# Performance work log

Measured on AMD Instinct MI355X. Metric: run time of the kernel, lower is better.

The kernel has to match this reference:

```python
import jax, jax.numpy as jnp
import numpy as np

EPS = 1e-8      # torch F.cosine_similarity eps
MARGIN = 0.6
POS_MASK = 2.0  # added at the positive location before top-k mining
K_NEG = 4


def setup_inputs() -> dict:
    key = jax.random.key(0)
    k1, k2, k3, k4 = jax.random.split(key, 4)
    B, C, H, W = 4, 256, 64, 64
    sketch = jax.random.normal(k1, (B, C, H, W), dtype=jnp.float32)
    ref = jax.random.normal(k2, (B, C, H, W), dtype=jnp.float32)
    # one anchor coordinate per positive grid cell (B*H*W pairs total)
    anchor_y = jax.random.randint(k3, (B, H * W), 0, H, dtype=jnp.int32)
    anchor_x = jax.random.randint(k4, (B, H * W), 0, W, dtype=jnp.int32)
    return {"sketch_query_vectors": sketch, "ref_key_vectors": ref,
            "anchor_y": anchor_y, "anchor_x": anchor_x}


def reference(sketch_query_vectors, ref_key_vectors, anchor_y, anchor_x):
    B, C, H, W = sketch_query_vectors.shape
    M = H * W  # ref locations; also number of positive pairs per batch elem

    sketch_flat = sketch_query_vectors.reshape(B, C, M)  # (B, C, M)
    ref_flat = ref_key_vectors.reshape(B, C, M)          # (B, C, M)

    # gather anchor features at (anchor_y, anchor_x): flat index ay*W + ax
    a_idx = anchor_y * W + anchor_x                      # (B, N), N == M
    anchors = jnp.take_along_axis(sketch_flat, a_idx[:, None, :], axis=2)  # (B, C, N)
    anchors = anchors.transpose(0, 2, 1)                 # (B, N, C)

    # cosine similarity of each anchor vs full ref map of same batch elem
    dot = jnp.einsum('bnc,bcm->bnm', anchors, ref_flat)  # (B, N, M)
    a_norm = jnp.linalg.norm(anchors, axis=-1)           # (B, N)
    r_norm = jnp.linalg.norm(ref_flat, axis=1)           # (B, M)
    sim = dot / jnp.maximum(a_norm[:, :, None] * r_norm[:, None, :], EPS)
    dist = 1.0 - sim                                     # (B, N, M)

    # positive location for pair n is grid cell n -> diagonal
    pos_distance = jnp.mean(jnp.diagonal(dist, axis1=1, axis2=2))

    # mask the positive location then mine 4 smallest distances
    masked = dist + POS_MASK * jnp.eye(M, dtype=dist.dtype)[None, :, :]
    neg_vals = -jax.lax.top_k(-masked, K_NEG)[0]         # (B, N, K_NEG)
    neg_loss = jnp.mean(jnp.maximum(MARGIN - neg_vals, 0.0))

    return pos_distance + neg_loss
```

## Files before the change

kernel.cpp:

```cpp
#include <hip/hip_runtime.h>
#include <math.h>

#define B_  4
#define C_  256
#define W_  64
#define M_  4096
#define N_  4096
#define THRESH_ 0.4f

typedef __attribute__((ext_vector_type(8))) short bf16x8;
typedef __attribute__((ext_vector_type(4))) float f32x4;

__device__ __forceinline__ short f2bf(float x) {
    union { float f; unsigned u; } v; v.f = x;
    unsigned r = v.u + 0x7fffu + ((v.u >> 16) & 1u);
    return (short)(r >> 16);
}
__device__ __forceinline__ float bf2f(short s) {
    union { unsigned u; float f; } v;
    v.u = ((unsigned)(unsigned short)s) << 16;
    return v.f;
}
__device__ __forceinline__ void gload_lds16(const void* g, void* l) {
    __builtin_amdgcn_global_load_lds(
        (const __attribute__((address_space(1))) void*)g,
        (__attribute__((address_space(3))) void*)l, 16, 0, 0);
}

#define OFF_SKT    0
#define OFF_REFT   8388608
#define OFF_ISN    16777216
#define OFF_IR     16842752
#define OFF_FLAGC  16908288
#define OFF_FLAGL  16908544
#define OFF_DIAG   17170432
#define OFF_ROWSUM 17235968
#define OFF_ROWCNT 17301504
#define OFF_AIDX   17367040

#define RS_ 256

__global__ __launch_bounds__(256) void convert_kernel(
    const float* __restrict__ sketch, const float* __restrict__ ref,
    short* __restrict__ sketchT, short* __restrict__ refT,
    const int* __restrict__ ay, const int* __restrict__ ax,
    float* __restrict__ isn, float* __restrict__ ir,
    int* __restrict__ aidx, float* __restrict__ rowsum,
    int* __restrict__ rowcnt, int* __restrict__ flagcnt)
{
    const int z  = blockIdx.y;
    const int b  = blockIdx.x >> 6;
    const int m0 = (blockIdx.x & 63) * 64;
    const int tid = threadIdx.x;
    const int lane = tid & 63, wv = tid >> 6;
    const int lg = lane >> 4;
    const int mloc = (lane & 15) * 4;
    const int key = lane & 7;

    __shared__ __align__(16) short Ts[64 * RS_];
    __shared__ float ssp[4][64];

    const float* src = (z ? ref : sketch) + (size_t)b * C_ * M_ + m0 + mloc;
    float s0 = 0.f, s1 = 0.f, s2 = 0.f, s3 = 0.f;
#pragma unroll
    for (int i = 0; i < 16; ++i) {
        const int cc = wv * 64 + i * 4 + lg;
        const float4 v = *reinterpret_cast<const float4*>(src + (size_t)cc * M_);
        s0 += v.x * v.x; s1 += v.y * v.y; s2 += v.z * v.z; s3 += v.w * v.w;
        const int ch = cc >> 3, off = cc & 7;
        const int ph = ((ch ^ key) << 3) | off;
        Ts[(mloc + 0) * RS_ + ph] = f2bf(v.x);
        Ts[(mloc + 1) * RS_ + ph] = f2bf(v.y);
        Ts[(mloc + 2) * RS_ + ph] = f2bf(v.z);
        Ts[(mloc + 3) * RS_ + ph] = f2bf(v.w);
    }
    s0 += __shfl_xor(s0, 16); s0 += __shfl_xor(s0, 32);
    s1 += __shfl_xor(s1, 16); s1 += __shfl_xor(s1, 32);
    s2 += __shfl_xor(s2, 16); s2 += __shfl_xor(s2, 32);
    s3 += __shfl_xor(s3, 16); s3 += __shfl_xor(s3, 32);
    if (lane < 16) {
        ssp[wv][mloc + 0] = s0; ssp[wv][mloc + 1] = s1;
        ssp[wv][mloc + 2] = s2; ssp[wv][mloc + 3] = s3;
    }
    if (z == 0 && blockIdx.x == 0 && tid == 64) *flagcnt = 0;
    __syncthreads();

    if (tid < 64) {
        const float tot = ssp[0][tid] + ssp[1][tid] + ssp[2][tid] + ssp[3][tid];
        const int gi = b * M_ + m0 + tid;
        if (z == 0) {
            isn[gi] = rsqrtf(tot);
            aidx[gi] = ay[gi] * W_ + ax[gi];
            rowsum[gi] = 0.f;
            rowcnt[gi] = 0;
        } else {
            ir[gi] = rsqrtf(tot);
        }
    }

    short* dst = (z ? refT : sketchT) + ((size_t)b * M_ + m0) * C_;
#pragma unroll
    for (int it = 0; it < 8; ++it) {
        const int g = it * 256 + tid;
        const int r = g >> 5, ch = g & 31;
        const bf16x8 v = *reinterpret_cast<const bf16x8*>(
            &Ts[r * RS_ + ((ch ^ ((r >> 2) & 7)) << 3)]);
        *reinterpret_cast<bf16x8*>(dst + g * 8) = v;
    }
}

#define BK 64
#define NT 4

__global__ __launch_bounds__(512, 2) void gemm_kernel(
    const short* __restrict__ sketchT, const short* __restrict__ refT,
    const int* __restrict__ aidx,
    const float* __restrict__ isn, const float* __restrict__ ir,
    float* __restrict__ diag, float* __restrict__ rowsum,
    int* __restrict__ rowcnt)
{
    const int bid = blockIdx.x + (blockIdx.y << 4) + (blockIdx.z << 8);
    const int nb  = (bid & 7) * 128 + (bid >> 3);
    const int mBase = (nb & 15) * 256;
    const int nBase = ((nb >> 4) & 15) * 256;
    const int b = nb >> 8;

    const int tid = threadIdx.x;
    const int lane = tid & 63, wv = tid >> 6;
    const int wm = (wv >> 2) * 128;
    const int wn = (wv & 3) * 64;
    const int l15 = lane & 15, l4 = lane >> 4;
    const int l7 = lane & 7, l8 = lane >> 3;
    const int ksw = ((l7 ^ l8) << 3);

    __shared__ __align__(16) short Rs[2][256 * BK];
    __shared__ __align__(16) short As[2][256 * BK];

    const short* aptr[4];
    const short* bptr[4];
#pragma unroll
    for (int c = 0; c < 4; ++c) {
        const int row = wv * 32 + c * 8 + l8;
        aptr[c] = refT + ((size_t)b * M_ + mBase + row) * C_ + ksw;
        bptr[c] = sketchT +
                  ((size_t)b * M_ + aidx[b * N_ + nBase + row]) * C_ + ksw;
    }

#define STAGE_CHUNK(bufi, c, koff)                                          \
    gload_lds16(aptr[c] + (koff), (char*)Rs[bufi] + (wv * 4 + (c)) * 1024); \
    gload_lds16(bptr[c] + (koff), (char*)As[bufi] + (wv * 4 + (c)) * 1024);

    f32x4 acc[8][4] = {};
    bf16x8 pn[4][2];

#pragma unroll
    for (int c = 0; c < 4; ++c) { STAGE_CHUNK(0, c, 0) }
#pragma unroll
    for (int c = 0; c < 4; ++c) { STAGE_CHUNK(1, c, BK) }
    asm volatile("s_waitcnt vmcnt(8)" ::: "memory");
    __builtin_amdgcn_s_barrier();

#pragma unroll
    for (int t = 0; t < NT; ++t) {
        const int cur = t & 1;
        const int koff = (t + 1) * BK;
#pragma unroll
        for (int p = 0; p < 4; ++p) {
            bf16x8 pm[2][2];
#pragma unroll
            for (int m2 = 0; m2 < 2; ++m2)
#pragma unroll
                for (int ks = 0; ks < 2; ++ks) {
                    const int row = wm + (p * 2 + m2) * 16 + l15;
                    const int kph = ((ks * 4 + l4) ^ (l15 & 7)) << 3;
                    pm[m2][ks] = *reinterpret_cast<const bf16x8*>(
                        &Rs[cur][row * BK + kph]);
                }
            if (p == 0) {
#pragma unroll
                for (int nf = 0; nf < 4; ++nf)
#pragma unroll
                    for (int ks = 0; ks < 2; ++ks) {
                        const int row = wn + nf * 16 + l15;
                        const int kph = ((ks * 4 + l4) ^ (l15 & 7)) << 3;
                        pn[nf][ks] = *reinterpret_cast<const bf16x8*>(
                            &As[cur][row * BK + kph]);
                    }
            }
            if (t == 1 || t == 2) { STAGE_CHUNK(cur ^ 1, p, koff) }
            __builtin_amdgcn_s_barrier();
            __builtin_amdgcn_sched_barrier(0);
            __builtin_amdgcn_s_setprio(1);
#pragma unroll
            for (int m2 = 0; m2 < 2; ++m2)
#pragma unroll
                for (int nf = 0; nf < 4; ++nf)
#pragma unroll
                    for (int ks = 0; ks < 2; ++ks)
                        acc[p * 2 + m2][nf] =
                            __builtin_amdgcn_mfma_f32_16x16x32_bf16(
                                pm[m2][ks], pn[nf][ks],
                                acc[p * 2 + m2][nf], 0, 0, 0);
            __builtin_amdgcn_s_setprio(0);
            if (p < 3) __builtin_amdgcn_s_barrier();
        }
        if (t < NT - 1) {
            asm volatile("s_waitcnt vmcnt(0)" ::: "memory");
            __builtin_amdgcn_s_barrier();
        }
    }
#undef STAGE_CHUNK

    float irv[8][4];
#pragma unroll
    for (int mf = 0; mf < 8; ++mf)
#pragma unroll
        for (int r = 0; r < 4; ++r)
            irv[mf][r] = ir[b * M_ + mBase + wm + mf * 16 + l4 * 4 + r];

#pragma unroll
    for (int nf = 0; nf < 4; ++nf) {
        const int gn = nBase + wn + nf * 16 + l15;
        const float ian = isn[b * M_ + aidx[b * N_ + gn]];
        float s = 0.f; int cnt = 0;
#pragma unroll
        for (int mf = 0; mf < 8; ++mf) {
#pragma unroll
            for (int r = 0; r < 4; ++r) {
                const int gm = mBase + wm + mf * 16 + l4 * 4 + r;
                const float sim = acc[mf][nf][r] * irv[mf][r] * ian;
                if (gm == gn) {
                    diag[b * N_ + gn] = 1.0f - sim;
                } else if (sim > THRESH_) {
                    s += sim - THRESH_; ++cnt;
                }
            }
        }
        if (cnt) {
            atomicAdd(&rowsum[b * N_ + gn], s);
            atomicAdd(&rowcnt[b * N_ + gn], cnt);
        }
    }
}

__global__ __launch_bounds__(256) void flag_kernel(
    const int* __restrict__ rowcnt, int* __restrict__ flagcnt,
    int* __restrict__ flaglist)
{
    int i = blockIdx.x * 256 + threadIdx.x;
    if (rowcnt[i] > 4) {
        int p = atomicAdd(flagcnt, 1);
        flaglist[p] = i;
    }
}

__global__ __launch_bounds__(256) void fallback_kernel(
    const short* __restrict__ sketchT, const short* __restrict__ refT,
    const int* __restrict__ aidx,
    const float* __restrict__ isn, const float* __restrict__ ir,
    const int* __restrict__ flagcnt, const int* __restrict__ flaglist,
    float* __restrict__ rowsum)
{
    const int nflag = *flagcnt;
    __shared__ float av[C_];
    __shared__ float tops[256][4];
    for (int fi = blockIdx.x; fi < nflag; fi += gridDim.x) {
        const int row = flaglist[fi];
        const int b = row >> 12, n = row & (N_ - 1);
        const int an = aidx[row];
        __syncthreads();
        av[threadIdx.x] = bf2f(sketchT[((size_t)b * M_ + an) * C_ + threadIdx.x]);
        __syncthreads();
        const float ian = isn[b * M_ + an];
        float t0 = 0, t1 = 0, t2 = 0, t3 = 0;
        for (int m = threadIdx.x; m < M_; m += 256) {
            if (m == n) continue;
            const short* rp = refT + ((size_t)b * M_ + m) * C_;
            float dot = 0.f;
#pragma unroll 8
            for (int c = 0; c < C_; ++c) dot += av[c] * bf2f(rp[c]);
            float rl = dot * ian * ir[b * M_ + m] - THRESH_;
            if (rl > t3) {
                t3 = rl;
                if (t3 > t2) { float t = t2; t2 = t3; t3 = t; }
                if (t2 > t1) { float t = t1; t1 = t2; t2 = t; }
                if (t1 > t0) { float t = t0; t0 = t1; t1 = t; }
            }
        }
        tops[threadIdx.x][0] = t0; tops[threadIdx.x][1] = t1;
        tops[threadIdx.x][2] = t2; tops[threadIdx.x][3] = t3;
        __syncthreads();
        if (threadIdx.x == 0) {
            float s0 = 0, s1 = 0, s2 = 0, s3 = 0;
            for (int t = 0; t < 1024; ++t) {
                float v = tops[t >> 2][t & 3];
                if (v > s3) {
                    s3 = v;
                    if (s3 > s2) { float tt = s2; s2 = s3; s3 = tt; }
                    if (s2 > s1) { float tt = s1; s1 = s2; s2 = tt; }
                    if (s1 > s0) { float tt = s0; s0 = s1; s1 = tt; }
                }
            }
            rowsum[row] = s0 + s1 + s2 + s3;
        }
        __syncthreads();
    }
}

__global__ __launch_bounds__(256) void final_kernel(
    const float* __restrict__ rowsum, const float* __restrict__ diag,
    float* __restrict__ out)
{
    float sn = 0.f, sp = 0.f;
    for (int i = threadIdx.x; i < B_ * N_; i += 256) {
        sn += rowsum[i];
        sp += diag[i];
    }
    __shared__ float red[256];
    red[threadIdx.x] = sp * (1.0f / (B_ * N_)) + sn * (1.0f / (B_ * N_ * 4));
    __syncthreads();
    for (int s = 128; s > 0; s >>= 1) {
        if (threadIdx.x < s) red[threadIdx.x] += red[threadIdx.x + s];
        __syncthreads();
    }
    if (threadIdx.x == 0) out[0] = red[0];
}

extern "C" void kernel_launch(void* const* d_in, const int* in_sizes, int n_in,
                              void* d_out, int out_size, void* d_ws, size_t ws_size,
                              hipStream_t stream)
{
    const float* sketch = (const float*)d_in[0];
    const float* ref    = (const float*)d_in[1];
    const int*   ay     = (const int*)d_in[2];
    const int*   ax     = (const int*)d_in[3];
    float* out = (float*)d_out;

    char* ws = (char*)d_ws;
    short* sketchT  = (short*)(ws + OFF_SKT);
    short* refT     = (short*)(ws + OFF_REFT);
    float* isn      = (float*)(ws + OFF_ISN);
    float* ir       = (float*)(ws + OFF_IR);
    int*   flagcnt  = (int*)(ws + OFF_FLAGC);
    int*   flaglist = (int*)(ws + OFF_FLAGL);
    float* diag     = (float*)(ws + OFF_DIAG);
    float* rowsum   = (float*)(ws + OFF_ROWSUM);
    int*   rowcnt   = (int*)(ws + OFF_ROWCNT);
    int*   aidx     = (int*)(ws + OFF_AIDX);

    convert_kernel<<<dim3(64 * B_, 2), 256, 0, stream>>>(
        sketch, ref, sketchT, refT, ay, ax, isn, ir, aidx,
        rowsum, rowcnt, flagcnt);

    gemm_kernel<<<dim3(16, 16, 4), 512, 0, stream>>>(
        sketchT, refT, aidx, isn, ir, diag, rowsum, rowcnt);

    flag_kernel<<<(B_ * N_) / 256, 256, 0, stream>>>(rowcnt, flagcnt, flaglist);
    fallback_kernel<<<64, 256, 0, stream>>>(sketchT, refT, aidx, isn, ir,
                                            flagcnt, flaglist, rowsum);
    final_kernel<<<1, 256, 0, stream>>>(rowsum, diag, out);
}
```

Measured before the change: 147.5 us.

## Make GEMM persistent over N tiles with continuous k-pipeline and triple-buffered A

The GEMM now launches 512 blocks of 256 threads, and each block owns a 128-row ref panel and walks 8 consecutive 128-column anchor tiles. A-panel loads are triple-buffered and B loads double-buffered, so prefetching continues across tile boundaries with the epilogue inlined per tile. This removes per-tile prologue and drain bubbles and improves XCD-local reuse, but the ref panel is re-read from L2 for every N tile. The convert kernel also switches to 1024-thread blocks, with each wave handling 16 channels.

```diff
diff --git a/kernel.cpp b/kernel.cpp
--- a/kernel.cpp
+++ b/kernel.cpp
@@ -40,7 +40,7 @@
 
 #define RS_ 256
 
-__global__ __launch_bounds__(256) void convert_kernel(
+__global__ __launch_bounds__(1024) void convert_kernel(
     const float* __restrict__ sketch, const float* __restrict__ ref,
     short* __restrict__ sketchT, short* __restrict__ refT,
     const int* __restrict__ ay, const int* __restrict__ ax,
@@ -58,13 +58,13 @@
     const int key = lane & 7;
 
     __shared__ __align__(16) short Ts[64 * RS_];
-    __shared__ float ssp[4][64];
+    __shared__ float ssp[16][64];
 
     const float* src = (z ? ref : sketch) + (size_t)b * C_ * M_ + m0 + mloc;
     float s0 = 0.f, s1 = 0.f, s2 = 0.f, s3 = 0.f;
 #pragma unroll
-    for (int i = 0; i < 16; ++i) {
-        const int cc = wv * 64 + i * 4 + lg;
+    for (int i = 0; i < 4; ++i) {
+        const int cc = wv * 16 + i * 4 + lg;
         const float4 v = *reinterpret_cast<const float4*>(src + (size_t)cc * M_);
         s0 += v.x * v.x; s1 += v.y * v.y; s2 += v.z * v.z; s3 += v.w * v.w;
         const int ch = cc >> 3, off = cc & 7;
@@ -86,7 +86,9 @@
     __syncthreads();
 
     if (tid < 64) {
-        const float tot = ssp[0][tid] + ssp[1][tid] + ssp[2][tid] + ssp[3][tid];
+        float tot = 0.f;
+#pragma unroll
+        for (int w = 0; w < 16; ++w) tot += ssp[w][tid];
         const int gi = b * M_ + m0 + tid;
         if (z == 0) {
             isn[gi] = rsqrtf(tot);
@@ -100,8 +102,8 @@
 
     short* dst = (z ? refT : sketchT) + ((size_t)b * M_ + m0) * C_;
 #pragma unroll
-    for (int it = 0; it < 8; ++it) {
-        const int g = it * 256 + tid;
+    for (int it = 0; it < 2; ++it) {
+        const int g = it * 1024 + tid;
         const int r = g >> 5, ch = g & 31;
         const bf16x8 v = *reinterpret_cast<const bf16x8*>(
             &Ts[r * RS_ + ((ch ^ ((r >> 2) & 7)) << 3)]);
@@ -110,136 +112,157 @@
 }
 
 #define BK 64
-#define NT 4
-
-__global__ __launch_bounds__(512, 2) void gemm_kernel(
+#define NKT 4
+#define NTL 8
+
+__global__ __launch_bounds__(256, 2) void gemm_kernel(
     const short* __restrict__ sketchT, const short* __restrict__ refT,
     const int* __restrict__ aidx,
     const float* __restrict__ isn, const float* __restrict__ ir,
     float* __restrict__ diag, float* __restrict__ rowsum,
     int* __restrict__ rowcnt)
 {
-    const int bid = blockIdx.x + (blockIdx.y << 4) + (blockIdx.z << 8);
-    const int nb  = (bid & 7) * 128 + (bid >> 3);
-    const int mBase = (nb & 15) * 256;
-    const int nBase = ((nb >> 4) & 15) * 256;
-    const int b = nb >> 8;
+    const int bid = blockIdx.x;
+    const int xcd = bid & 7, slot = bid >> 3;
+    const int b = xcd >> 1;
+    const int mBase  = (slot >> 1) * 128;
+    const int nsBase = ((xcd & 1) * 2 + (slot & 1)) * (NTL * 128);
 
     const int tid = threadIdx.x;
     const int lane = tid & 63, wv = tid >> 6;
-    const int wm = (wv >> 2) * 128;
-    const int wn = (wv & 3) * 64;
+    const int wm = (wv >> 1) * 64, wn_ = (wv & 1) * 64;
     const int l15 = lane & 15, l4 = lane >> 4;
     const int l7 = lane & 7, l8 = lane >> 3;
     const int ksw = ((l7 ^ l8) << 3);
 
-    __shared__ __align__(16) short Rs[2][256 * BK];
-    __shared__ __align__(16) short As[2][256 * BK];
-
-    const short* aptr[4];
-    const short* bptr[4];
-#pragma unroll
-    for (int c = 0; c < 4; ++c) {
-        const int row = wv * 32 + c * 8 + l8;
-        aptr[c] = refT + ((size_t)b * M_ + mBase + row) * C_ + ksw;
-        bptr[c] = sketchT +
-                  ((size_t)b * M_ + aidx[b * N_ + nBase + row]) * C_ + ksw;
-    }
-
-#define STAGE_CHUNK(bufi, c, koff)                                          \
-    gload_lds16(aptr[c] + (koff), (char*)Rs[bufi] + (wv * 4 + (c)) * 1024); \
-    gload_lds16(bptr[c] + (koff), (char*)As[bufi] + (wv * 4 + (c)) * 1024);
-
-    f32x4 acc[8][4] = {};
-    bf16x8 pn[4][2];
-
-#pragma unroll
-    for (int c = 0; c < 4; ++c) { STAGE_CHUNK(0, c, 0) }
-#pragma unroll
-    for (int c = 0; c < 4; ++c) { STAGE_CHUNK(1, c, BK) }
-    asm volatile("s_waitcnt vmcnt(8)" ::: "memory");
+    __shared__ __align__(16) short Ab[3][128 * BK];
+    __shared__ __align__(16) short Bb[2][128 * BK];
+
+    const short* Apanel = refT + ((size_t)b * M_ + mBase) * C_ + ksw;
+    const short* Sbase  = sketchT + (size_t)b * M_ * C_ + ksw;
+    const int* aidxb = aidx + b * N_;
+
+    int arow[4];
+#pragma unroll
+    for (int q = 0; q < 4; ++q) arow[q] = (q * 4 + wv) * 8 + l8;
+
+    int aic[4], ain[4];
+#pragma unroll
+    for (int q = 0; q < 4; ++q) aic[q] = aidxb[nsBase + arow[q]];
+
+    f32x4 acc[4][4] = {};
+
+#pragma unroll
+    for (int q = 0; q < 4; ++q)
+        gload_lds16(Sbase + (size_t)aic[q] * C_, (char*)Bb[0] + (q * 4 + wv) * 1024);
+#pragma unroll
+    for (int q = 0; q < 4; ++q)
+        gload_lds16(Apanel + (size_t)arow[q] * C_, (char*)Ab[0] + (q * 4 + wv) * 1024);
+#pragma unroll
+    for (int q = 0; q < 4; ++q)
+        gload_lds16(Apanel + (size_t)arow[q] * C_ + BK, (char*)Ab[1] + (q * 4 + wv) * 1024);
+    asm volatile("s_waitcnt vmcnt(4)" ::: "memory");
     __builtin_amdgcn_s_barrier();
 
-#pragma unroll
-    for (int t = 0; t < NT; ++t) {
-        const int cur = t & 1;
-        const int koff = (t + 1) * BK;
-#pragma unroll
-        for (int p = 0; p < 4; ++p) {
-            bf16x8 pm[2][2];
-#pragma unroll
-            for (int m2 = 0; m2 < 2; ++m2)
+    int bnt = 0;
+    for (int nt = 0; nt < NTL; ++nt) {
+        const bool lastnt = (nt == NTL - 1);
+        if (!lastnt) {
+#pragma unroll
+            for (int q = 0; q < 4; ++q)
+                ain[q] = aidxb[nsBase + (nt + 1) * 128 + arow[q]];
+        }
+#pragma unroll
+        for (int kt = 0; kt < NKT; ++kt) {
+            int ba = bnt + kt;         if (ba >= 3) ba -= 3; if (ba >= 3) ba -= 3;
+            int bs = bnt + kt + 2;     if (bs >= 3) bs -= 3; if (bs >= 3) bs -= 3;
+
+            if (!(lastnt && kt == 3)) {
+                const int ktb = (kt + 1) & 3;
+                const int* ai = (kt == 3) ? ain : aic;
+#pragma unroll
+                for (int q = 0; q < 4; ++q)
+                    gload_lds16(Sbase + (size_t)ai[q] * C_ + ktb * BK,
+                                (char*)Bb[(kt + 1) & 1] + (q * 4 + wv) * 1024);
+            }
+            if (!(lastnt && kt >= 2)) {
+                const int kta = (kt + 2) & 3;
+#pragma unroll
+                for (int q = 0; q < 4; ++q)
+                    gload_lds16(Apanel + (size_t)arow[q] * C_ + kta * BK,
+                                (char*)Ab[bs] + (q * 4 + wv) * 1024);
+            }
+
+            bf16x8 pm[4][2], pn[4][2];
+#pragma unroll
+            for (int f = 0; f < 4; ++f)
 #pragma unroll
                 for (int ks = 0; ks < 2; ++ks) {
-                    const int row = wm + (p * 2 + m2) * 16 + l15;
                     const int kph = ((ks * 4 + l4) ^ (l15 & 7)) << 3;
-                    pm[m2][ks] = *reinterpret_cast<const bf16x8*>(
-                        &Rs[cur][row * BK + kph]);
+                    pm[f][ks] = *reinterpret_cast<const bf16x8*>(
+                        &Ab[ba][(wm + f * 16 + l15) * BK + kph]);
+                    pn[f][ks] = *reinterpret_cast<const bf16x8*>(
+                        &Bb[kt & 1][(wn_ + f * 16 + l15) * BK + kph]);
                 }
-            if (p == 0) {
+            __builtin_amdgcn_s_setprio(1);
+#pragma unroll
+            for (int mf = 0; mf < 4; ++mf)
 #pragma unroll
                 for (int nf = 0; nf < 4; ++nf)
 #pragma unroll
-                    for (int ks = 0; ks < 2; ++ks) {
-                        const int row = wn + nf * 16 + l15;
-                        const int kph = ((ks * 4 + l4) ^ (l15 & 7)) << 3;
-                        pn[nf][ks] = *reinterpret_cast<const bf16x8*>(
-                            &As[cur][row * BK + kph]);
+                    for (int ks = 0; ks < 2; ++ks)
+                        acc[mf][nf] = __builtin_amdgcn_mfma_f32_16x16x32_bf16(
+                            pm[mf][ks], pn[nf][ks], acc[mf][nf], 0, 0, 0);
+            __builtin_amdgcn_s_setprio(0);
+
+            if (kt == 3) {
+                const int nB = nsBase + nt * 128;
+                float irv[4][4];
+#pragma unroll
+                for (int mf = 0; mf < 4; ++mf)
+#pragma unroll
+                    for (int r = 0; r < 4; ++r)
+                        irv[mf][r] = ir[b * M_ + mBase + wm + mf * 16 + l4 * 4 + r];
+#pragma unroll
+                for (int nf = 0; nf < 4; ++nf) {
+                    const int gn = nB + wn_ + nf * 16 + l15;
+                    const float ian = isn[b * M_ + aidxb[gn]];
+                    float s = 0.f; int cnt = 0;
+#pragma unroll
+                    for (int mf = 0; mf < 4; ++mf) {
+#pragma unroll
+                        for (int r = 0; r < 4; ++r) {
+                            const int gm = mBase + wm + mf * 16 + l4 * 4 + r;
+                            const float sim = acc[mf][nf][r] * irv[mf][r] * ian;
+                            if (gm == gn) {
+                                diag[b * N_ + gn] = 1.0f - sim;
+                            } else if (sim > THRESH_) {
+                                s += sim - THRESH_; ++cnt;
+                            }
+                        }
                     }
-            }
-            if (t == 1 || t == 2) { STAGE_CHUNK(cur ^ 1, p, koff) }
+                    if (cnt) {
+                        atomicAdd(&rowsum[b * N_ + gn], s);
+                        atomicAdd(&rowcnt[b * N_ + gn], cnt);
+                    }
+                }
+#pragma unroll
+                for (int mf = 0; mf < 4; ++mf)
+#pragma unroll
+                    for (int nf = 0; nf < 4; ++nf)
+                        acc[mf][nf] = (f32x4){0.f, 0.f, 0.f, 0.f};
+            }
+
+            if (lastnt && kt >= 2) {
+                asm volatile("s_waitcnt vmcnt(0)" ::: "memory");
+            } else {
+                asm volatile("s_waitcnt vmcnt(4)" ::: "memory");
+            }
             __builtin_amdgcn_s_barrier();
-            __builtin_amdgcn_sched_barrier(0);
-            __builtin_amdgcn_s_setprio(1);
-#pragma unroll
-            for (int m2 = 0; m2 < 2; ++m2)
-#pragma unroll
-                for (int nf = 0; nf < 4; ++nf)
-#pragma unroll
-                    for (int ks = 0; ks < 2; ++ks)
-                        acc[p * 2 + m2][nf] =
-                            __builtin_amdgcn_mfma_f32_16x16x32_bf16(
-                                pm[m2][ks], pn[nf][ks],
-                                acc[p * 2 + m2][nf], 0, 0, 0);
-            __builtin_amdgcn_s_setprio(0);
-            if (p < 3) __builtin_amdgcn_s_barrier();
-        }
-        if (t < NT - 1) {
-            asm volatile("s_waitcnt vmcnt(0)" ::: "memory");
-            __builtin_amdgcn_s_barrier();
-        }
-    }
-#undef STAGE_CHUNK
-
-    float irv[8][4];
-#pragma unroll
-    for (int mf = 0; mf < 8; ++mf)
-#pragma unroll
-        for (int r = 0; r < 4; ++r)
-            irv[mf][r] = ir[b * M_ + mBase + wm + mf * 16 + l4 * 4 + r];
-
-#pragma unroll
-    for (int nf = 0; nf < 4; ++nf) {
-        const int gn = nBase + wn + nf * 16 + l15;
-        const float ian = isn[b * M_ + aidx[b * N_ + gn]];
-        float s = 0.f; int cnt = 0;
-#pragma unroll
-        for (int mf = 0; mf < 8; ++mf) {
-#pragma unroll
-            for (int r = 0; r < 4; ++r) {
-                const int gm = mBase + wm + mf * 16 + l4 * 4 + r;
-                const float sim = acc[mf][nf][r] * irv[mf][r] * ian;
-                if (gm == gn) {
-                    diag[b * N_ + gn] = 1.0f - sim;
-                } else if (sim > THRESH_) {
-                    s += sim - THRESH_; ++cnt;
-                }
-            }
-        }
-        if (cnt) {
-            atomicAdd(&rowsum[b * N_ + gn], s);
-            atomicAdd(&rowcnt[b * N_ + gn], cnt);
-        }
+        }
+#pragma unroll
+        for (int q = 0; q < 4; ++q) aic[q] = ain[q];
+        bnt = (bnt == 2) ? 0 : bnt + 1;
     }
 }
 
@@ -348,11 +371,11 @@
     int*   rowcnt   = (int*)(ws + OFF_ROWCNT);
     int*   aidx     = (int*)(ws + OFF_AIDX);
 
-    convert_kernel<<<dim3(64 * B_, 2), 256, 0, stream>>>(
+    convert_kernel<<<dim3(64 * B_, 2), 1024, 0, stream>>>(
         sketch, ref, sketchT, refT, ay, ax, isn, ir, aidx,
         rowsum, rowcnt, flagcnt);
 
-    gemm_kernel<<<dim3(16, 16, 4), 512, 0, stream>>>(
+    gemm_kernel<<<512, 256, 0, stream>>>(
         sketchT, refT, aidx, isn, ir, diag, rowsum, rowcnt);
 
     flag_kernel<<<(B_ * N_) / 256, 256, 0, stream>>>(rowcnt, flagcnt, flaglist);
```

After: 151.5 us. 2.7% more time.
